# Optimization experiments

Hardware: AMD Instinct MI355X
Metric: run time of the kernel (lower is better)

The kernel has to match this reference:

```python
import jax, jax.numpy as jnp
import numpy as np

KERNEL = 7
STRIDE = 3
C_IN, C_OUT = 3, 4
HIDDEN, OUTPUT = 64, 10
H_OUT = (32 - KERNEL) // STRIDE + 1  # 9
FC1_IN = C_OUT * H_OUT * H_OUT       # 324


def setup_inputs() -> dict:
    key = jax.random.key(0)
    ks = jax.random.split(key, 6)
    B = 16384
    x = jax.random.normal(ks[0], (B, C_IN, 32, 32), dtype=jnp.float32)
    conv_w = jax.random.normal(ks[1], (C_OUT, C_IN, KERNEL, KERNEL), dtype=jnp.float32) * 0.05
    fc1_w = jax.random.normal(ks[2], (HIDDEN, FC1_IN), dtype=jnp.float32) * (1.0 / np.sqrt(FC1_IN))
    fc1_b = jax.random.normal(ks[3], (HIDDEN,), dtype=jnp.float32) * 0.01
    fc2_w = jax.random.normal(ks[4], (OUTPUT, HIDDEN), dtype=jnp.float32) * (1.0 / np.sqrt(HIDDEN))
    fc2_b = jax.random.normal(ks[5], (OUTPUT,), dtype=jnp.float32) * 0.01
    return {"x": x, "conv_w": conv_w, "fc1_w": fc1_w, "fc1_b": fc1_b, "fc2_w": fc2_w, "fc2_b": fc2_b}


def reference(x, conv_w, fc1_w, fc1_b, fc2_w, fc2_b):
    # conv (NO bias, matching original forward which only uses conv1.weight)
    y = jax.lax.conv_general_dilated(
        x, conv_w, window_strides=(STRIDE, STRIDE), padding='VALID',
        dimension_numbers=('NCHW', 'OIHW', 'NCHW'))  # [B, 4, 9, 9]
    y = y * y
    y = y.reshape(y.shape[0], -1)                    # [B, 324]
    h = y @ fc1_w.T + fc1_b                          # [B, 64]
    h = h * h
    out = h @ fc2_w.T + fc2_b                        # [B, 10]
    return out
```

## Files before the change

kernel.cpp:

```cpp
#include <hip/hip_runtime.h>
#include <string.h>


typedef _Float16 f16;
typedef f16 f16x8 __attribute__((ext_vector_type(8)));
typedef __fp16 fp16x2 __attribute__((ext_vector_type(2)));
typedef float f32x4 __attribute__((ext_vector_type(4)));

#define WIN_B  13824
#define YS_B   27648
#define LDS_B  (27648 + 11520)

__device__ __forceinline__ unsigned pack_rtz(float a, float b) {
    fp16x2 h = __builtin_amdgcn_cvt_pkrtz(a, b);
    unsigned u; memcpy(&u, &h, 4); return u;
}

__device__ __forceinline__ void write_windows(f16* wptr, const unsigned h[16]) {
#pragma unroll
    for (int ow = 0; ow < 9; ow += 2) {
        int d = (3 * ow) >> 1;
        uint4 v; v.x = h[d]; v.y = h[d+1]; v.z = h[d+2]; v.w = h[d+3];
        *reinterpret_cast<uint4*>(wptr + ow * 8) = v;
    }
#pragma unroll
    for (int ow = 1; ow < 9; ow += 2) {
        int d = (3 * ow) >> 1;
        uint4 v;
        v.x = __builtin_amdgcn_alignbit(h[d+1], h[d],   16);
        v.y = __builtin_amdgcn_alignbit(h[d+2], h[d+1], 16);
        v.z = __builtin_amdgcn_alignbit(h[d+3], h[d+2], 16);
        v.w = __builtin_amdgcn_alignbit(h[d+4], h[d+3], 16);
        *reinterpret_cast<uint4*>(wptr + ow * 8) = v;
    }
}

__global__ __launch_bounds__(256, 4) void convnet_mfma(
    const float* __restrict__ x,
    const float* __restrict__ cw,
    const float* __restrict__ fc1w,
    const float* __restrict__ fc1b,
    const float* __restrict__ fc2w,
    const float* __restrict__ fc2b,
    float* __restrict__ out)
{
    __shared__ unsigned char lds[LDS_B];
    f16* YS   = (f16*)(lds + YS_B);
    float* HSQ = (float*)lds;

    const int t    = threadIdx.x;
    const int lane = t & 63;
    const int w    = t >> 6;
    const int g    = lane >> 4;
    const int lr   = lane & 15;
    const size_t base_s = (size_t)blockIdx.x * 16;

    f16x8 wcf[6];
#pragma unroll
    for (int st = 0; st < 6; ++st) {
        f16x8 v = {0, 0, 0, 0, 0, 0, 0, 0};
        int seg = st * 4 + g;
        if (lr < 4 && seg <= 20) {
            int ci = seg >= 14 ? 2 : (seg >= 7 ? 1 : 0);
            int kh = seg - ci * 7;
            const float* wr = cw + ((lr * 3 + ci) * 7 + kh) * 7;
#pragma unroll
            for (int j = 0; j < 7; ++j) v[j] = (f16)wr[j];
        }
        wcf[st] = v;
    }

    int seg2off[6];
#pragma unroll
    for (int st = 0; st < 6; ++st) {
        int seg  = st * 4 + g;
        int segc = seg > 20 ? 20 : seg;
        int ci   = segc >= 14 ? 2 : (segc >= 7 ? 1 : 0);
        int kh   = segc - ci * 7;
        seg2off[st] = ci * 4608 + kh * 144;
    }

    const int ntiles = (w >= 2) ? 2 : 1;
    const int tileA  = (w == 0) ? 2 : (w == 1) ? 5 : (w == 2) ? 0 : 1;
    const int tileB  = (w == 2) ? 3 : 4;
    int rowbase[2], pbase[2];
#pragma unroll
    for (int ti = 0; ti < 2; ++ti) {
        int tc   = ti ? tileB : tileA;
        int grow = tc * 16 + lr;
        int p    = grow > 80 ? 80 : grow;
        int oh   = (p * 57) >> 9;
        int ow   = p - oh * 9;
        rowbase[ti] = oh * 432 + ow * 16;
        pbase[ti]   = tc * 16 + g * 4;
    }

    const bool stg  = t < 96;
    const int  sci  = t >> 5;
    const int  srow = t & 31;
    const int  goff = sci * 1024 + srow * 32;
    const int  woff = sci * 2304 + srow * 72;

    float4 ldv[8];
    unsigned hh[16];
    if (stg) {
        const float* gp = x + base_s * 3072 + goff;
#pragma unroll
        for (int i = 0; i < 8; ++i) ldv[i] = *(const float4*)(gp + 4 * i);
    }
#pragma unroll
    for (int i = 0; i < 2; ++i) {
        int idx = i * 256 + t;
        if (idx < 288) {
            int si = idx / 18, d = idx - si * 18;
            *(unsigned*)(YS + si * 360 + 324 + d * 2) = 0u;
        }
    }
    if (stg) {
#pragma unroll
        for (int i = 0; i < 8; ++i) {
            hh[2*i]   = pack_rtz(ldv[i].x, ldv[i].y);
            hh[2*i+1] = pack_rtz(ldv[i].z, ldv[i].w);
        }
        write_windows((f16*)(lds) + woff, hh);
        const float* gp = x + (base_s + 1) * 3072 + goff;
#pragma unroll
        for (int i = 0; i < 8; ++i) ldv[i] = *(const float4*)(gp + 4 * i);
    }
    __syncthreads();

    for (int s = 0; s < 16; ++s) {
        const unsigned char* winb = lds + (s & 1) * WIN_B;
        f16* wino = (f16*)(lds + ((s & 1) ^ 1) * WIN_B);
        f16* ysp  = YS + s * 360;

        __builtin_amdgcn_s_setprio(1);
#pragma unroll
        for (int ti = 0; ti < 2; ++ti) {
            if (ti < ntiles) {
                const unsigned char* pA = winb + rowbase[ti];
                f32x4 acc = {0.f, 0.f, 0.f, 0.f};
#pragma unroll
                for (int st = 0; st < 6; ++st) {
                    f16x8 af = *(const f16x8*)(pA + seg2off[st]);
                    acc = __builtin_amdgcn_mfma_f32_16x16x32_f16(af, wcf[st], acc, 0, 0, 0);
                }
                if (lr < 4) {
#pragma unroll
                    for (int r = 0; r < 4; ++r) {
                        int p = pbase[ti] + r;
                        if (p < 81) {
                            float y = acc[r];
                            ysp[lr * 81 + p] = (f16)(y * y);
                        }
                    }
                }
            }
        }
        __builtin_amdgcn_s_setprio(0);

        if (s < 15 && stg) {
#pragma unroll
            for (int i = 0; i < 8; ++i) {
                hh[2*i]   = pack_rtz(ldv[i].x, ldv[i].y);
                hh[2*i+1] = pack_rtz(ldv[i].z, ldv[i].w);
            }
            write_windows(wino + woff, hh);
        }
        if (s < 14 && stg) {
            const float* gp = x + (base_s + s + 2) * 3072 + goff;
#pragma unroll
            for (int i = 0; i < 8; ++i) ldv[i] = *(const float4*)(gp + 4 * i);
        }
        __syncthreads();
    }

    {
        f32x4 a1 = {0.f, 0.f, 0.f, 0.f};
        const int n = w * 16 + lr;
        const float* w1r = fc1w + n * 324;
        __builtin_amdgcn_s_setprio(1);
#pragma unroll
        for (int st = 0; st < 10; ++st) {
            f16x8 av = *(const f16x8*)(YS + lr * 360 + st * 32 + g * 8);
            float4 v0 = *(const float4*)(w1r + st * 32 + g * 8);
            float4 v1 = *(const float4*)(w1r + st * 32 + g * 8 + 4);
            float vv[8] = {v0.x, v0.y, v0.z, v0.w, v1.x, v1.y, v1.z, v1.w};
            f16x8 bh, bl;
#pragma unroll
            for (int j = 0; j < 8; ++j) {
                f16 hi = (f16)vv[j];
                bh[j] = hi;
                bl[j] = (f16)(vv[j] - (float)hi);
            }
            a1 = __builtin_amdgcn_mfma_f32_16x16x32_f16(av, bh, a1, 0, 0, 0);
            a1 = __builtin_amdgcn_mfma_f32_16x16x32_f16(av, bl, a1, 0, 0, 0);
        }
        {
            f16x8 av = *(const f16x8*)(YS + lr * 360 + 320 + g * 8);
            f16x8 bh = {0,0,0,0,0,0,0,0}, bl = {0,0,0,0,0,0,0,0};
            if (g == 0) {
                float4 v0 = *(const float4*)(w1r + 320);
                float vv[4] = {v0.x, v0.y, v0.z, v0.w};
#pragma unroll
                for (int j = 0; j < 4; ++j) {
                    f16 hi = (f16)vv[j];
                    bh[j] = hi;
                    bl[j] = (f16)(vv[j] - (float)hi);
                }
            }
            a1 = __builtin_amdgcn_mfma_f32_16x16x32_f16(av, bh, a1, 0, 0, 0);
            a1 = __builtin_amdgcn_mfma_f32_16x16x32_f16(av, bl, a1, 0, 0, 0);
        }
        __builtin_amdgcn_s_setprio(0);
        float bias = fc1b[n];
#pragma unroll
        for (int r = 0; r < 4; ++r) {
            int s = g * 4 + r;
            float h = a1[r] + bias;
            HSQ[s * 65 + n] = h * h;
        }
    }
    __syncthreads();

    if (t < 160) {
        int sj = t / 10, j = t - sj * 10;
        float a = fc2b[j];
        const float* wr = fc2w + j * 64;
        const float* hv = &HSQ[sj * 65];
#pragma unroll
        for (int i = 0; i < 64; ++i) a += wr[i] * hv[i];
        out[(base_s + sj) * 10 + j] = a;
    }
}

extern "C" void kernel_launch(void* const* d_in, const int* in_sizes, int n_in,
                              void* d_out, int out_size, void* d_ws, size_t ws_size,
                              hipStream_t stream) {
    const float* x    = (const float*)d_in[0];
    const float* cw   = (const float*)d_in[1];
    const float* fc1w = (const float*)d_in[2];
    const float* fc1b = (const float*)d_in[3];
    const float* fc2w = (const float*)d_in[4];
    const float* fc2b = (const float*)d_in[5];
    float* out = (float*)d_out;

    const int B = in_sizes[0] / 3072;
    hipLaunchKernelGGL(convnet_mfma, dim3(B / 16), dim3(256), 0, stream,
                       x, cw, fc1w, fc1b, fc2w, fc2b, out);
}
```

Before: 45.98 us.

## Process 32 samples per block to amortize fc1 weight loads

Doubles the samples handled per block from 16 to 32, so each block converts the fc1 weights to split fp16 once and runs the MFMAs for two 16-sample row tiles with them. This halves the number of blocks and the per-block fixed overhead: weight fragment setup, fc1 weight global reads and the conversion work. In exchange LDS use grows and the launch-bounds occupancy hint drops from 4 to 2 blocks per CU. With half as many blocks, the serial conv loop per block is twice as long, which lowers parallelism and reduces latency hiding on the memory-bound input stream.

```diff
diff --git a/kernel.cpp b/kernel.cpp
--- a/kernel.cpp
+++ b/kernel.cpp
@@ -7,9 +7,10 @@
 typedef __fp16 fp16x2 __attribute__((ext_vector_type(2)));
 typedef float f32x4 __attribute__((ext_vector_type(4)));
 
+#define NS     32
 #define WIN_B  13824
 #define YS_B   27648
-#define LDS_B  (27648 + 11520)
+#define LDS_B  (27648 + NS * 720)
 
 __device__ __forceinline__ unsigned pack_rtz(float a, float b) {
     fp16x2 h = __builtin_amdgcn_cvt_pkrtz(a, b);
@@ -35,7 +36,7 @@
     }
 }
 
-__global__ __launch_bounds__(256, 4) void convnet_mfma(
+__global__ __launch_bounds__(256, 2) void convnet_mfma(
     const float* __restrict__ x,
     const float* __restrict__ cw,
     const float* __restrict__ fc1w,
@@ -53,7 +54,7 @@
     const int w    = t >> 6;
     const int g    = lane >> 4;
     const int lr   = lane & 15;
-    const size_t base_s = (size_t)blockIdx.x * 16;
+    const size_t base_s = (size_t)blockIdx.x * NS;
 
     f16x8 wcf[6];
 #pragma unroll
@@ -109,9 +110,9 @@
         for (int i = 0; i < 8; ++i) ldv[i] = *(const float4*)(gp + 4 * i);
     }
 #pragma unroll
-    for (int i = 0; i < 2; ++i) {
+    for (int i = 0; i < 3; ++i) {
         int idx = i * 256 + t;
-        if (idx < 288) {
+        if (idx < NS * 18) {
             int si = idx / 18, d = idx - si * 18;
             *(unsigned*)(YS + si * 360 + 324 + d * 2) = 0u;
         }
@@ -129,7 +130,7 @@
     }
     __syncthreads();
 
-    for (int s = 0; s < 16; ++s) {
+    for (int s = 0; s < NS; ++s) {
         const unsigned char* winb = lds + (s & 1) * WIN_B;
         f16* wino = (f16*)(lds + ((s & 1) ^ 1) * WIN_B);
         f16* ysp  = YS + s * 360;
@@ -159,7 +160,7 @@
         }
         __builtin_amdgcn_s_setprio(0);
 
-        if (s < 15 && stg) {
+        if (s < NS - 1 && stg) {
 #pragma unroll
             for (int i = 0; i < 8; ++i) {
                 hh[2*i]   = pack_rtz(ldv[i].x, ldv[i].y);
@@ -167,7 +168,7 @@
             }
             write_windows(wino + woff, hh);
         }
-        if (s < 14 && stg) {
+        if (s < NS - 2 && stg) {
             const float* gp = x + (base_s + s + 2) * 3072 + goff;
 #pragma unroll
             for (int i = 0; i < 8; ++i) ldv[i] = *(const float4*)(gp + 4 * i);
@@ -176,13 +177,15 @@
     }
 
     {
+        f32x4 a0 = {0.f, 0.f, 0.f, 0.f};
         f32x4 a1 = {0.f, 0.f, 0.f, 0.f};
         const int n = w * 16 + lr;
         const float* w1r = fc1w + n * 324;
         __builtin_amdgcn_s_setprio(1);
 #pragma unroll
         for (int st = 0; st < 10; ++st) {
-            f16x8 av = *(const f16x8*)(YS + lr * 360 + st * 32 + g * 8);
+            f16x8 av0 = *(const f16x8*)(YS +        lr  * 360 + st * 32 + g * 8);
+            f16x8 av1 = *(const f16x8*)(YS + (16 + lr) * 360 + st * 32 + g * 8);
             float4 v0 = *(const float4*)(w1r + st * 32 + g * 8);
             float4 v1 = *(const float4*)(w1r + st * 32 + g * 8 + 4);
             float vv[8] = {v0.x, v0.y, v0.z, v0.w, v1.x, v1.y, v1.z, v1.w};
@@ -193,11 +196,14 @@
                 bh[j] = hi;
                 bl[j] = (f16)(vv[j] - (float)hi);
             }
-            a1 = __builtin_amdgcn_mfma_f32_16x16x32_f16(av, bh, a1, 0, 0, 0);
-            a1 = __builtin_amdgcn_mfma_f32_16x16x32_f16(av, bl, a1, 0, 0, 0);
+            a0 = __builtin_amdgcn_mfma_f32_16x16x32_f16(av0, bh, a0, 0, 0, 0);
+            a0 = __builtin_amdgcn_mfma_f32_16x16x32_f16(av0, bl, a0, 0, 0, 0);
+            a1 = __builtin_amdgcn_mfma_f32_16x16x32_f16(av1, bh, a1, 0, 0, 0);
+            a1 = __builtin_amdgcn_mfma_f32_16x16x32_f16(av1, bl, a1, 0, 0, 0);
         }
         {
-            f16x8 av = *(const f16x8*)(YS + lr * 360 + 320 + g * 8);
+            f16x8 av0 = *(const f16x8*)(YS +        lr  * 360 + 320 + g * 8);
+            f16x8 av1 = *(const f16x8*)(YS + (16 + lr) * 360 + 320 + g * 8);
             f16x8 bh = {0,0,0,0,0,0,0,0}, bl = {0,0,0,0,0,0,0,0};
             if (g == 0) {
                 float4 v0 = *(const float4*)(w1r + 320);
@@ -209,28 +215,36 @@
                     bl[j] = (f16)(vv[j] - (float)hi);
                 }
             }
-            a1 = __builtin_amdgcn_mfma_f32_16x16x32_f16(av, bh, a1, 0, 0, 0);
-            a1 = __builtin_amdgcn_mfma_f32_16x16x32_f16(av, bl, a1, 0, 0, 0);
+            a0 = __builtin_amdgcn_mfma_f32_16x16x32_f16(av0, bh, a0, 0, 0, 0);
+            a0 = __builtin_amdgcn_mfma_f32_16x16x32_f16(av0, bl, a0, 0, 0, 0);
+            a1 = __builtin_amdgcn_mfma_f32_16x16x32_f16(av1, bh, a1, 0, 0, 0);
+            a1 = __builtin_amdgcn_mfma_f32_16x16x32_f16(av1, bl, a1, 0, 0, 0);
         }
         __builtin_amdgcn_s_setprio(0);
         float bias = fc1b[n];
 #pragma unroll
         for (int r = 0; r < 4; ++r) {
-            int s = g * 4 + r;
-            float h = a1[r] + bias;
-            HSQ[s * 65 + n] = h * h;
+            int s0 = g * 4 + r;
+            float h0 = a0[r] + bias;
+            HSQ[s0 * 65 + n] = h0 * h0;
+            float h1 = a1[r] + bias;
+            HSQ[(s0 + 16) * 65 + n] = h1 * h1;
         }
     }
     __syncthreads();
 
-    if (t < 160) {
-        int sj = t / 10, j = t - sj * 10;
-        float a = fc2b[j];
-        const float* wr = fc2w + j * 64;
-        const float* hv = &HSQ[sj * 65];
-#pragma unroll
-        for (int i = 0; i < 64; ++i) a += wr[i] * hv[i];
-        out[(base_s + sj) * 10 + j] = a;
+#pragma unroll
+    for (int b = 0; b < 2; ++b) {
+        int idx = b * 256 + t;
+        if (idx < NS * 10) {
+            int sj = idx / 10, j = idx - sj * 10;
+            float a = fc2b[j];
+            const float* wr = fc2w + j * 64;
+            const float* hv = &HSQ[sj * 65];
+#pragma unroll
+            for (int i = 0; i < 64; ++i) a += wr[i] * hv[i];
+            out[(base_s + sj) * 10 + j] = a;
+        }
     }
 }
 
@@ -246,6 +260,6 @@
     float* out = (float*)d_out;
 
     const int B = in_sizes[0] / 3072;
-    hipLaunchKernelGGL(convnet_mfma, dim3(B / 16), dim3(256), 0, stream,
+    hipLaunchKernelGGL(convnet_mfma, dim3(B / NS), dim3(256), 0, stream,
                        x, cw, fc1w, fc1b, fc2w, fc2b, out);
 }
```

Result: faster. 41.75 us (-9.2%).

## Use 512-thread blocks with warp-specialized staging and one conv tile per wave

Applied to the files above, without the earlier changes.

Each block now handles 32 samples with 8 waves. Waves 0-1 only stage input windows and waves 2-7 each compute one conv tile, so staging and MFMA work are split across dedicated warps. FC1 work is spread over two 16-sample M-tiles. The aim is to overlap global loads and packing with conv MFMAs and to balance tiles across waves. In exchange the block needs more LDS, the grid has half as many blocks, and the per-sample loop is twice as long.

```diff
diff --git a/kernel.cpp b/kernel.cpp
--- a/kernel.cpp
+++ b/kernel.cpp
@@ -7,9 +7,10 @@
 typedef __fp16 fp16x2 __attribute__((ext_vector_type(2)));
 typedef float f32x4 __attribute__((ext_vector_type(4)));
 
+#define NS     32
 #define WIN_B  13824
 #define YS_B   27648
-#define LDS_B  (27648 + 11520)
+#define LDS_B  (27648 + NS * 720)
 
 __device__ __forceinline__ unsigned pack_rtz(float a, float b) {
     fp16x2 h = __builtin_amdgcn_cvt_pkrtz(a, b);
@@ -35,7 +36,7 @@
     }
 }
 
-__global__ __launch_bounds__(256, 4) void convnet_mfma(
+__global__ __launch_bounds__(512, 4) void convnet_mfma(
     const float* __restrict__ x,
     const float* __restrict__ cw,
     const float* __restrict__ fc1w,
@@ -53,7 +54,7 @@
     const int w    = t >> 6;
     const int g    = lane >> 4;
     const int lr   = lane & 15;
-    const size_t base_s = (size_t)blockIdx.x * 16;
+    const size_t base_s = (size_t)blockIdx.x * NS;
 
     f16x8 wcf[6];
 #pragma unroll
@@ -80,19 +81,16 @@
         seg2off[st] = ci * 4608 + kh * 144;
     }
 
-    const int ntiles = (w >= 2) ? 2 : 1;
-    const int tileA  = (w == 0) ? 2 : (w == 1) ? 5 : (w == 2) ? 0 : 1;
-    const int tileB  = (w == 2) ? 3 : 4;
-    int rowbase[2], pbase[2];
-#pragma unroll
-    for (int ti = 0; ti < 2; ++ti) {
-        int tc   = ti ? tileB : tileA;
+    const bool has_tile = (w >= 2);
+    const int  tc = has_tile ? (w - 2) : 0;
+    int rowbase, pbase;
+    {
         int grow = tc * 16 + lr;
         int p    = grow > 80 ? 80 : grow;
         int oh   = (p * 57) >> 9;
         int ow   = p - oh * 9;
-        rowbase[ti] = oh * 432 + ow * 16;
-        pbase[ti]   = tc * 16 + g * 4;
+        rowbase = oh * 432 + ow * 16;
+        pbase   = tc * 16 + g * 4;
     }
 
     const bool stg  = t < 96;
@@ -110,8 +108,8 @@
     }
 #pragma unroll
     for (int i = 0; i < 2; ++i) {
-        int idx = i * 256 + t;
-        if (idx < 288) {
+        int idx = i * 512 + t;
+        if (idx < NS * 18) {
             int si = idx / 18, d = idx - si * 18;
             *(unsigned*)(YS + si * 360 + 324 + d * 2) = 0u;
         }
@@ -129,60 +127,60 @@
     }
     __syncthreads();
 
-    for (int s = 0; s < 16; ++s) {
+    for (int s = 0; s < NS; ++s) {
         const unsigned char* winb = lds + (s & 1) * WIN_B;
         f16* wino = (f16*)(lds + ((s & 1) ^ 1) * WIN_B);
         f16* ysp  = YS + s * 360;
 
-        __builtin_amdgcn_s_setprio(1);
-#pragma unroll
-        for (int ti = 0; ti < 2; ++ti) {
-            if (ti < ntiles) {
-                const unsigned char* pA = winb + rowbase[ti];
-                f32x4 acc = {0.f, 0.f, 0.f, 0.f};
-#pragma unroll
-                for (int st = 0; st < 6; ++st) {
-                    f16x8 af = *(const f16x8*)(pA + seg2off[st]);
-                    acc = __builtin_amdgcn_mfma_f32_16x16x32_f16(af, wcf[st], acc, 0, 0, 0);
-                }
-                if (lr < 4) {
-#pragma unroll
-                    for (int r = 0; r < 4; ++r) {
-                        int p = pbase[ti] + r;
-                        if (p < 81) {
-                            float y = acc[r];
-                            ysp[lr * 81 + p] = (f16)(y * y);
-                        }
+        if (has_tile) {
+            __builtin_amdgcn_s_setprio(1);
+            const unsigned char* pA = winb + rowbase;
+            f32x4 acc = {0.f, 0.f, 0.f, 0.f};
+#pragma unroll
+            for (int st = 0; st < 6; ++st) {
+                f16x8 af = *(const f16x8*)(pA + seg2off[st]);
+                acc = __builtin_amdgcn_mfma_f32_16x16x32_f16(af, wcf[st], acc, 0, 0, 0);
+            }
+            __builtin_amdgcn_s_setprio(0);
+            if (lr < 4) {
+#pragma unroll
+                for (int r = 0; r < 4; ++r) {
+                    int p = pbase + r;
+                    if (p < 81) {
+                        float y = acc[r];
+                        ysp[lr * 81 + p] = (f16)(y * y);
                     }
                 }
             }
-        }
-        __builtin_amdgcn_s_setprio(0);
-
-        if (s < 15 && stg) {
-#pragma unroll
-            for (int i = 0; i < 8; ++i) {
-                hh[2*i]   = pack_rtz(ldv[i].x, ldv[i].y);
-                hh[2*i+1] = pack_rtz(ldv[i].z, ldv[i].w);
-            }
-            write_windows(wino + woff, hh);
-        }
-        if (s < 14 && stg) {
-            const float* gp = x + (base_s + s + 2) * 3072 + goff;
-#pragma unroll
-            for (int i = 0; i < 8; ++i) ldv[i] = *(const float4*)(gp + 4 * i);
+        } else {
+            if (s < NS - 1 && stg) {
+#pragma unroll
+                for (int i = 0; i < 8; ++i) {
+                    hh[2*i]   = pack_rtz(ldv[i].x, ldv[i].y);
+                    hh[2*i+1] = pack_rtz(ldv[i].z, ldv[i].w);
+                }
+                write_windows(wino + woff, hh);
+            }
+            if (s < NS - 2 && stg) {
+                const float* gp = x + (base_s + s + 2) * 3072 + goff;
+#pragma unroll
+                for (int i = 0; i < 8; ++i) ldv[i] = *(const float4*)(gp + 4 * i);
+            }
         }
         __syncthreads();
     }
 
     {
         f32x4 a1 = {0.f, 0.f, 0.f, 0.f};
-        const int n = w * 16 + lr;
+        const int mt = w >> 2;
+        const int mw = w & 3;
+        const int n  = mw * 16 + lr;
         const float* w1r = fc1w + n * 324;
+        const f16* ysrow = YS + (mt * 16 + lr) * 360;
         __builtin_amdgcn_s_setprio(1);
 #pragma unroll
         for (int st = 0; st < 10; ++st) {
-            f16x8 av = *(const f16x8*)(YS + lr * 360 + st * 32 + g * 8);
+            f16x8 av = *(const f16x8*)(ysrow + st * 32 + g * 8);
             float4 v0 = *(const float4*)(w1r + st * 32 + g * 8);
             float4 v1 = *(const float4*)(w1r + st * 32 + g * 8 + 4);
             float vv[8] = {v0.x, v0.y, v0.z, v0.w, v1.x, v1.y, v1.z, v1.w};
@@ -197,7 +195,7 @@
             a1 = __builtin_amdgcn_mfma_f32_16x16x32_f16(av, bl, a1, 0, 0, 0);
         }
         {
-            f16x8 av = *(const f16x8*)(YS + lr * 360 + 320 + g * 8);
+            f16x8 av = *(const f16x8*)(ysrow + 320 + g * 8);
             f16x8 bh = {0,0,0,0,0,0,0,0}, bl = {0,0,0,0,0,0,0,0};
             if (g == 0) {
                 float4 v0 = *(const float4*)(w1r + 320);
@@ -216,14 +214,14 @@
         float bias = fc1b[n];
 #pragma unroll
         for (int r = 0; r < 4; ++r) {
-            int s = g * 4 + r;
+            int s0 = mt * 16 + g * 4 + r;
             float h = a1[r] + bias;
-            HSQ[s * 65 + n] = h * h;
+            HSQ[s0 * 65 + n] = h * h;
         }
     }
     __syncthreads();
 
-    if (t < 160) {
+    if (t < NS * 10) {
         int sj = t / 10, j = t - sj * 10;
         float a = fc2b[j];
         const float* wr = fc2w + j * 64;
@@ -246,6 +244,6 @@
     float* out = (float*)d_out;
 
     const int B = in_sizes[0] / 3072;
-    hipLaunchKernelGGL(convnet_mfma, dim3(B / 16), dim3(256), 0, stream,
+    hipLaunchKernelGGL(convnet_mfma, dim3(B / NS), dim3(512), 0, stream,
                        x, cw, fc1w, fc1b, fc2w, fc2b, out);
 }
```

Result: faster. 44.16 us (-4.0%).
